# Optimization experiments

Measured on AMD Instinct MI355X. Metric: run time of the kernel, lower is better.

## Reference

```python
import jax, jax.numpy as jnp
import numpy as np

N = 100000
E = 1600000
C_IN = 128
C_OUT = 128
EPS = 1e-5


def setup_inputs() -> dict:
    key = jax.random.key(0)
    ks = jax.random.split(key, 8)
    x = jax.random.normal(ks[0], (N, C_IN), dtype=jnp.float32)
    edge_index = jax.random.randint(ks[1], (2, E), 0, N, dtype=jnp.int64)
    s_proj = 1.0 / np.sqrt(C_IN)
    s_out = 1.0 / np.sqrt(C_IN)
    W_proj = jax.random.uniform(ks[2], (C_IN, C_IN), jnp.float32, -s_proj, s_proj)
    b_proj = jax.random.uniform(ks[3], (C_IN,), jnp.float32, -s_proj, s_proj)
    W_l = jax.random.uniform(ks[4], (C_OUT, C_IN), jnp.float32, -s_out, s_out)
    b_l = jax.random.uniform(ks[5], (C_OUT,), jnp.float32, -s_out, s_out)
    W_r = jax.random.uniform(ks[6], (C_OUT, C_IN), jnp.float32, -s_out, s_out)
    gamma = jnp.ones((C_OUT,), jnp.float32)
    beta = jnp.zeros((C_OUT,), jnp.float32)
    return {"x": x, "edge_index": edge_index, "W_proj": W_proj, "b_proj": b_proj,
            "W_l": W_l, "b_l": b_l, "W_r": W_r, "gamma": gamma, "beta": beta}


def reference(x, edge_index, W_proj, b_proj, W_l, b_l, W_r, gamma, beta):
    # SAGEConv(project=True, aggr='sum'): project+ReLU source features per node,
    # gather along edges, scatter-sum at targets, then lin_l(agg) + lin_r(x_root).
    src, dst = edge_index[0], edge_index[1]
    h = jax.nn.relu(x @ W_proj.T + b_proj)            # [N, C_IN]
    msg = h[src]                                       # [E, C_IN] edge gather
    agg = jax.ops.segment_sum(msg, dst, num_segments=N)  # [N, C_IN]
    out = agg @ W_l.T + b_l + x @ W_r.T                # [N, C_OUT] (root uses unprojected x)
    # LayerNorm(c_out)
    mu = jnp.mean(out, axis=-1, keepdims=True)
    var = jnp.var(out, axis=-1, keepdims=True)
    return (out - mu) * jax.lax.rsqrt(var + EPS) * gamma + beta
```

## Files before the change

kernel.cpp:

```cpp
#include <hip/hip_runtime.h>
#include <stdint.h>

#define NN 100000
#define NE 1600000
#define C  128
#define NB 782
#define CAP 4096
#define SB_SHIFT 13
#define MB 782
#define P1B 250

typedef __attribute__((ext_vector_type(8))) short short8;
typedef __attribute__((ext_vector_type(4))) float f32x4;

__device__ __forceinline__ float bf2f(uint16_t u) {
  union { uint32_t u; float f; } v; v.u = ((uint32_t)u) << 16; return v.f;
}
__device__ __forceinline__ uint16_t f2bf(float f) {
  union { float f; uint32_t u; } v; v.f = f;
  uint32_t r = v.u + 0x7fffu + ((v.u >> 16) & 1u);
  return (uint16_t)(r >> 16);
}

__global__ __launch_bounds__(256) void cast3_k(
    const float* __restrict__ a, const float* __restrict__ b, const float* __restrict__ c,
    uint16_t* __restrict__ oa, uint16_t* __restrict__ ob, uint16_t* __restrict__ oc)
{
  int i = blockIdx.x * 256 + threadIdx.x;
  int which = i >> 12, j = i & 4095;
  const float* s = which == 0 ? a : (which == 1 ? b : c);
  uint16_t* d    = which == 0 ? oa : (which == 1 ? ob : oc);
  float4 v = ((const float4*)s)[j];
  uint2 p;
  p.x = (uint32_t)f2bf(v.x) | ((uint32_t)f2bf(v.y) << 16);
  p.y = (uint32_t)f2bf(v.z) | ((uint32_t)f2bf(v.w) << 16);
  ((uint2*)d)[j] = p;
}


__global__ __launch_bounds__(512) void fused_front_k(
    const float* __restrict__ x, const uint16_t* __restrict__ wpb,
    const float* __restrict__ bias, uint16_t* __restrict__ h,
    uint16_t* __restrict__ xb,
    const int* __restrict__ esrc, const int* __restrict__ edst,
    int* __restrict__ gcnt, uint32_t* __restrict__ ebuf)
{
  extern __shared__ uint8_t slds[];
  const int t = threadIdx.x;

  if (blockIdx.x < MB) {
#pragma unroll
    for (int q = 0; q < 4; ++q) {
      int ci = q * 512 + t;
      int c = ci >> 4, k16 = ci & 15;
      *(short8*)(slds + c * 256 + ((k16 ^ (c & 15)) << 4)) =
          *(const short8*)(wpb + ci * 8);
    }
    __syncthreads();

    const int w = t >> 6, lane = t & 63;
    const int tile_m = blockIdx.x * 128 + w * 16;
    if (tile_m >= NN) return;
    const int r16 = lane & 15, g = lane >> 4;

    short8 a[4];
    const float* xp = x + (size_t)(tile_m + r16) * C + g * 8;
    uint16_t* xbp = xb + (size_t)(tile_m + r16) * C + g * 8;
#pragma unroll
    for (int kk = 0; kk < 4; ++kk) {
      float4 u = *(const float4*)(xp + kk * 32);
      float4 v = *(const float4*)(xp + kk * 32 + 4);
      short8 av;
      av[0] = (short)f2bf(u.x); av[1] = (short)f2bf(u.y);
      av[2] = (short)f2bf(u.z); av[3] = (short)f2bf(u.w);
      av[4] = (short)f2bf(v.x); av[5] = (short)f2bf(v.y);
      av[6] = (short)f2bf(v.z); av[7] = (short)f2bf(v.w);
      a[kk] = av;
      *(short8*)(xbp + kk * 32) = av;
    }

#pragma unroll
    for (int nt = 0; nt < 8; ++nt) {
      f32x4 acc = {0.f, 0.f, 0.f, 0.f};
      const int c = nt * 16 + r16;
      const uint8_t* rb = slds + c * 256;
#pragma unroll
      for (int kk = 0; kk < 4; ++kk) {
        short8 b = *(const short8*)(rb + ((((kk << 2) + g) ^ (c & 15)) << 4));
        acc = __builtin_amdgcn_mfma_f32_16x16x32_bf16(a[kk], b, acc, 0, 0, 0);
      }
      const float bv = bias[c];
#pragma unroll
      for (int r = 0; r < 4; ++r) {
        int row = tile_m + g * 4 + r;
        float v = acc[r] + bv;
        v = v > 0.f ? v : 0.f;
        h[(size_t)row * C + c] = f2bf(v);
      }
    }
  } else {
    int* bh = (int*)slds;
    int* gb = bh + NB;
    const int blk = blockIdx.x - MB;
    const int base = blk * 6400;

    for (int i = t; i < NB; i += 512) bh[i] = 0;

    const int4* ed4 = (const int4*)(edst + base);
    const int4* es4 = (const int4*)(esrc + base);
    int4 dv[4], sv[4];
    bool val[4];
#pragma unroll
    for (int k = 0; k < 4; ++k) {
      int i = t + k * 512;
      val[k] = (i < 1600);
      if (val[k]) { dv[k] = ed4[i]; sv[k] = es4[i]; }
    }
    __syncthreads();

#pragma unroll
    for (int k = 0; k < 4; ++k) if (val[k]) {
      atomicAdd(&bh[dv[k].x >> 7], 1); atomicAdd(&bh[dv[k].y >> 7], 1);
      atomicAdd(&bh[dv[k].z >> 7], 1); atomicAdd(&bh[dv[k].w >> 7], 1);
    }
    __syncthreads();

    for (int i = t; i < NB; i += 512) {
      int c = bh[i];
      gb[i] = c ? atomicAdd(&gcnt[i], c) : 0;
      bh[i] = 0;
    }
    __syncthreads();

#define P1_SCATTER(d, s) do { \
      int bb = (d) >> 7; \
      int o = atomicAdd(&bh[bb], 1); \
      int pos = gb[bb] + o; \
      if (pos < CAP) ebuf[(size_t)bb * CAP + pos] = ((uint32_t)((d) & 127) << 17) | (uint32_t)(s); \
    } while (0)

#pragma unroll
    for (int k = 0; k < 4; ++k) if (val[k]) {
      P1_SCATTER(dv[k].x, sv[k].x); P1_SCATTER(dv[k].y, sv[k].y);
      P1_SCATTER(dv[k].z, sv[k].z); P1_SCATTER(dv[k].w, sv[k].w);
    }
#undef P1_SCATTER
  }
}

__global__ __launch_bounds__(1024) void scan_block_k(
    const int* __restrict__ in, int* __restrict__ out, int n)
{
  __shared__ int sm[1024];
  int t = threadIdx.x;
  int v = (t < n) ? in[t] : 0;
  sm[t] = v;
  __syncthreads();
  for (int off = 1; off < 1024; off <<= 1) {
    int x = (t >= off) ? sm[t - off] : 0;
    __syncthreads();
    sm[t] += x;
    __syncthreads();
  }
  if (t < n) out[t] = sm[t] - v;
}

__global__ __launch_bounds__(256) void phase2_k(
    const uint32_t* __restrict__ ebuf, const int* __restrict__ gcnt,
    const int* __restrict__ gbase, int* __restrict__ ssrc,
    int* __restrict__ start, int* __restrict__ deg)
{
  __shared__ uint32_t raw[CAP];
  __shared__ int lout[CAP];
  __shared__ int cnt2[128 * 16];
  __shared__ int nd[128];
  const int b = blockIdx.x, t = threadIdx.x;
  const int n0 = b * 128;
  int cnt = gcnt[b]; if (cnt > CAP) cnt = CAP;
  const int base = gbase[b];

  for (int i = t; i < 128 * 16; i += 256) cnt2[i] = 0;
  __syncthreads();
  for (int i = t; i < cnt; i += 256) {
    uint32_t v = ebuf[(size_t)b * CAP + i];
    raw[i] = v;
    atomicAdd(&cnt2[(v >> 17) * 16 + ((v & 0x1FFFFu) >> SB_SHIFT)], 1);
  }
  __syncthreads();

  int deg_t = 0;
  if (t < 128) {
#pragma unroll
    for (int i = 0; i < 16; ++i) deg_t += cnt2[t * 16 + i];
    nd[t] = deg_t;
  }
  __syncthreads();
  for (int off = 1; off < 128; off <<= 1) {
    int v = 0;
    if (t < 128 && t >= off) v = nd[t - off];
    __syncthreads();
    if (t < 128) nd[t] += v;
    __syncthreads();
  }
  if (t < 128) {
    int pref = nd[t] - deg_t;
    if (n0 + t < NN) { start[n0 + t] = base + pref; deg[n0 + t] = deg_t; }
    int run = pref;
#pragma unroll
    for (int i = 0; i < 16; ++i) { int c = cnt2[t * 16 + i]; cnt2[t * 16 + i] = run; run += c; }
  }
  __syncthreads();
  for (int i = t; i < cnt; i += 256) {
    uint32_t v = raw[i];
    int o = atomicAdd(&cnt2[(v >> 17) * 16 + ((v & 0x1FFFFu) >> SB_SHIFT)], 1);
    lout[o] = (int)(v & 0x1FFFFu);
  }
  __syncthreads();
  for (int i = t; i < cnt; i += 256) ssrc[base + i] = lout[i];
}

__global__ __launch_bounds__(256) void aggregate_k(
    const uint16_t* __restrict__ h, const int* __restrict__ ssrc,
    const int* __restrict__ start, const int* __restrict__ deg,
    uint16_t* __restrict__ agg)
{
  const int wid = (blockIdx.x * 256 + threadIdx.x) >> 6;
  if (wid >= NN) return;
  const int lane = threadIdx.x & 63;
  const int q = lane >> 4;
  const int l16 = lane & 15;
  const int s0 = start[wid];
  const int cnt = deg[wid];
  const size_t choff = (size_t)l16 * 8;
  float a[8];
#pragma unroll
  for (int i = 0; i < 8; ++i) a[i] = 0.f;

#define ACC8(v) do { \
    a[0] += bf2f((uint16_t)(v).x); a[1] += bf2f((uint16_t)((v).x >> 16)); \
    a[2] += bf2f((uint16_t)(v).y); a[3] += bf2f((uint16_t)((v).y >> 16)); \
    a[4] += bf2f((uint16_t)(v).z); a[5] += bf2f((uint16_t)((v).z >> 16)); \
    a[6] += bf2f((uint16_t)(v).w); a[7] += bf2f((uint16_t)((v).w >> 16)); \
  } while (0)

  int j = 0;
  for (; j + 16 <= cnt; j += 16) {
    int e0 = ssrc[s0 + j + q];
    int e1 = ssrc[s0 + j + 4 + q];
    int e2 = ssrc[s0 + j + 8 + q];
    int e3 = ssrc[s0 + j + 12 + q];
    uint4 v0 = *(const uint4*)(h + (size_t)e0 * C + choff);
    uint4 v1 = *(const uint4*)(h + (size_t)e1 * C + choff);
    uint4 v2 = *(const uint4*)(h + (size_t)e2 * C + choff);
    uint4 v3 = *(const uint4*)(h + (size_t)e3 * C + choff);
    ACC8(v0); ACC8(v1); ACC8(v2); ACC8(v3);
  }
  const int rem = cnt - j;
  if (rem > 0) {
    int i0 = (q      < rem) ? q      : 0;
    int i1 = (q + 4  < rem) ? q + 4  : 0;
    int i2 = (q + 8  < rem) ? q + 8  : 0;
    int i3 = (q + 12 < rem) ? q + 12 : 0;
    int e0 = ssrc[s0 + j + i0];
    int e1 = ssrc[s0 + j + i1];
    int e2 = ssrc[s0 + j + i2];
    int e3 = ssrc[s0 + j + i3];
    uint4 v0 = *(const uint4*)(h + (size_t)e0 * C + choff);
    uint4 v1 = *(const uint4*)(h + (size_t)e1 * C + choff);
    uint4 v2 = *(const uint4*)(h + (size_t)e2 * C + choff);
    uint4 v3 = *(const uint4*)(h + (size_t)e3 * C + choff);
    if (q < rem)      ACC8(v0);
    if (q + 4 < rem)  ACC8(v1);
    if (q + 8 < rem)  ACC8(v2);
    if (q + 12 < rem) ACC8(v3);
  }
#undef ACC8

#pragma unroll
  for (int i = 0; i < 8; ++i) {
    a[i] += __shfl_xor(a[i], 16, 64);
    a[i] += __shfl_xor(a[i], 32, 64);
  }
  if (q == 0) {
    uint4 p;
    p.x = (uint32_t)f2bf(a[0]) | ((uint32_t)f2bf(a[1]) << 16);
    p.y = (uint32_t)f2bf(a[2]) | ((uint32_t)f2bf(a[3]) << 16);
    p.z = (uint32_t)f2bf(a[4]) | ((uint32_t)f2bf(a[5]) << 16);
    p.w = (uint32_t)f2bf(a[6]) | ((uint32_t)f2bf(a[7]) << 16);
    *(uint4*)(agg + (size_t)wid * C + choff) = p;
  }
}

__global__ __launch_bounds__(512) void gemm_out_k(
    const uint16_t* __restrict__ aggb, const uint16_t* __restrict__ xb,
    const uint16_t* __restrict__ wlb, const uint16_t* __restrict__ wrb,
    const float* __restrict__ bl, const float* __restrict__ gamma,
    const float* __restrict__ beta, float* __restrict__ out)
{
  extern __shared__ uint8_t slds[];
  const int t = threadIdx.x;
#pragma unroll
  for (int q = 0; q < 4; ++q) {
    int ci = q * 512 + t;
    int c = ci >> 4, k16 = ci & 15;
    *(short8*)(slds + c * 256 + ((k16 ^ (c & 15)) << 4)) =
        *(const short8*)(wlb + ci * 8);
  }
#pragma unroll
  for (int q = 0; q < 4; ++q) {
    int ci = q * 512 + t;
    int c = ci >> 4, k16 = ci & 15;
    *(short8*)(slds + 32768 + c * 256 + ((k16 ^ (c & 15)) << 4)) =
        *(const short8*)(wrb + ci * 8);
  }
  __syncthreads();

  const int w = t >> 6, lane = t & 63;
  const int tile_m = blockIdx.x * 128 + w * 16;
  if (tile_m >= NN) return;
  const int r16 = lane & 15, g = lane >> 4;

  short8 a0[4], a1[4];
  const uint16_t* p0 = aggb + (size_t)(tile_m + r16) * C + g * 8;
  const uint16_t* p1 = xb   + (size_t)(tile_m + r16) * C + g * 8;
#pragma unroll
  for (int kk = 0; kk < 4; ++kk) {
    a0[kk] = *(const short8*)(p0 + kk * 32);
    a1[kk] = *(const short8*)(p1 + kk * 32);
  }

  f32x4 acc[8];
#pragma unroll
  for (int nt = 0; nt < 8; ++nt) {
    f32x4 c4 = {0.f, 0.f, 0.f, 0.f};
    const int c = nt * 16 + r16;
    const uint8_t* rbl = slds + c * 256;
    const uint8_t* rbr = slds + 32768 + c * 256;
#pragma unroll
    for (int kk = 0; kk < 4; ++kk) {
      short8 b = *(const short8*)(rbl + ((((kk << 2) + g) ^ (c & 15)) << 4));
      c4 = __builtin_amdgcn_mfma_f32_16x16x32_bf16(a0[kk], b, c4, 0, 0, 0);
    }
#pragma unroll
    for (int kk = 0; kk < 4; ++kk) {
      short8 b = *(const short8*)(rbr + ((((kk << 2) + g) ^ (c & 15)) << 4));
      c4 = __builtin_amdgcn_mfma_f32_16x16x32_bf16(a1[kk], b, c4, 0, 0, 0);
    }
    const float bv = bl[c];
#pragma unroll
    for (int r = 0; r < 4; ++r) c4[r] += bv;
    acc[nt] = c4;
  }

  float s1[4], s2[4];
#pragma unroll
  for (int r = 0; r < 4; ++r) { s1[r] = 0.f; s2[r] = 0.f; }
#pragma unroll
  for (int nt = 0; nt < 8; ++nt)
#pragma unroll
    for (int r = 0; r < 4; ++r) { float v = acc[nt][r]; s1[r] += v; s2[r] += v * v; }
#pragma unroll
  for (int m = 1; m <= 8; m <<= 1) {
#pragma unroll
    for (int r = 0; r < 4; ++r) {
      s1[r] += __shfl_xor(s1[r], m, 64);
      s2[r] += __shfl_xor(s2[r], m, 64);
    }
  }
  float mean[4], rstd[4];
#pragma unroll
  for (int r = 0; r < 4; ++r) {
    mean[r] = s1[r] * (1.f / C);
    float var = s2[r] * (1.f / C) - mean[r] * mean[r];
    rstd[r] = rsqrtf(var + 1e-5f);
  }
#pragma unroll
  for (int nt = 0; nt < 8; ++nt) {
    const int col = nt * 16 + r16;
    const float gmv = gamma[col], btv = beta[col];
#pragma unroll
    for (int r = 0; r < 4; ++r) {
      int row = tile_m + g * 4 + r;
      out[(size_t)row * C + col] = (acc[nt][r] - mean[r]) * rstd[r] * gmv + btv;
    }
  }
}

extern "C" void kernel_launch(void* const* d_in, const int* in_sizes, int n_in,
                              void* d_out, int out_size, void* d_ws, size_t ws_size,
                              hipStream_t stream)
{
  const float* x        = (const float*)d_in[0];
  const int* ei         = (const int*)d_in[1];
  const float* Wp       = (const float*)d_in[2];
  const float* bp       = (const float*)d_in[3];
  const float* Wl       = (const float*)d_in[4];
  const float* bl       = (const float*)d_in[5];
  const float* Wr       = (const float*)d_in[6];
  const float* gamma    = (const float*)d_in[7];
  const float* beta     = (const float*)d_in[8];
  float* out            = (float*)d_out;

  char* ws = (char*)d_ws;
  uint16_t* xb   = (uint16_t*)(ws + 0);
  uint16_t* h    = (uint16_t*)(ws + 25600000);
  uint16_t* aggb = (uint16_t*)(ws + 51200000);
  uint32_t* ebuf = (uint32_t*)(ws + 51200000);
  uint16_t* wpb  = (uint16_t*)(ws + 76800000);
  uint16_t* wlb  = (uint16_t*)(ws + 76832768);
  uint16_t* wrb  = (uint16_t*)(ws + 76865536);
  int* deg       = (int*)(ws + 76898304);
  int* start     = (int*)(ws + 77298304);
  int* gcnt      = (int*)(ws + 77698304);
  int* gbase     = (int*)(ws + 77702400);
  int* ssrc      = (int*)(ws + 78102400);

  const int* esrc = ei;
  const int* edst = ei + NE;

  hipMemsetAsync(gcnt, 0, NB * sizeof(int), stream);

  cast3_k<<<48, 256, 0, stream>>>(Wp, Wl, Wr, wpb, wlb, wrb);

  fused_front_k<<<MB + P1B, 512, 32768, stream>>>(
      x, wpb, bp, h, xb, esrc, edst, gcnt, ebuf);

  scan_block_k<<<1, 1024, 0, stream>>>(gcnt, gbase, NB);
  phase2_k<<<NB, 256, 0, stream>>>(ebuf, gcnt, gbase, ssrc, start, deg);

  aggregate_k<<<(NN + 3) / 4, 256, 0, stream>>>(h, ssrc, start, deg, aggb);

  gemm_out_k<<<MB, 512, 65536, stream>>>(aggb, xb, wlb, wrb, bl, gamma, beta, out);
}
```

Baseline: 136.5 us.

## Fuse aggregation with output GEMM and move root projection into front kernel

The root term x@W_r^T+b_l now runs in the front kernel next to the projection, reusing the same x fragments, and is stored as a bf16 buffer in place of the bf16 copy of x. Aggregation and the lin_l GEMM with LayerNorm are merged into one kernel. Each wave gathers 16 rows into an LDS tile, with each 16-lane group handling one node and 8 neighbours in flight, then runs MFMA against W_l held in LDS. This removes the agg round trip through global memory and one launch. In exchange the gather parallelism per node changes, the front kernel needs 64KB LDS, and the root term is now rounded to bf16.

Result: slower. 175.2 us (+28.4%).

```diff
diff --git a/kernel.cpp b/kernel.cpp
--- a/kernel.cpp
+++ b/kernel.cpp
@@ -40,8 +40,9 @@
 
 __global__ __launch_bounds__(512) void fused_front_k(
     const float* __restrict__ x, const uint16_t* __restrict__ wpb,
-    const float* __restrict__ bias, uint16_t* __restrict__ h,
-    uint16_t* __restrict__ xb,
+    const uint16_t* __restrict__ wrb,
+    const float* __restrict__ bp, const float* __restrict__ bl,
+    uint16_t* __restrict__ h, uint16_t* __restrict__ rb,
     const int* __restrict__ esrc, const int* __restrict__ edst,
     int* __restrict__ gcnt, uint32_t* __restrict__ ebuf)
 {
@@ -50,11 +51,12 @@
 
   if (blockIdx.x < MB) {
 #pragma unroll
-    for (int q = 0; q < 4; ++q) {
-      int ci = q * 512 + t;
+    for (int qq = 0; qq < 4; ++qq) {
+      int ci = qq * 512 + t;
       int c = ci >> 4, k16 = ci & 15;
-      *(short8*)(slds + c * 256 + ((k16 ^ (c & 15)) << 4)) =
-          *(const short8*)(wpb + ci * 8);
+      int slot = (k16 ^ (c & 15)) << 4;
+      *(short8*)(slds + c * 256 + slot)         = *(const short8*)(wpb + ci * 8);
+      *(short8*)(slds + 32768 + c * 256 + slot) = *(const short8*)(wrb + ci * 8);
     }
     __syncthreads();
 
@@ -63,9 +65,9 @@
     if (tile_m >= NN) return;
     const int r16 = lane & 15, g = lane >> 4;
 
+    int arow = tile_m + r16; if (arow >= NN) arow = NN - 1;
     short8 a[4];
-    const float* xp = x + (size_t)(tile_m + r16) * C + g * 8;
-    uint16_t* xbp = xb + (size_t)(tile_m + r16) * C + g * 8;
+    const float* xp = x + (size_t)arow * C + g * 8;
 #pragma unroll
     for (int kk = 0; kk < 4; ++kk) {
       float4 u = *(const float4*)(xp + kk * 32);
@@ -76,26 +78,31 @@
       av[4] = (short)f2bf(v.x); av[5] = (short)f2bf(v.y);
       av[6] = (short)f2bf(v.z); av[7] = (short)f2bf(v.w);
       a[kk] = av;
-      *(short8*)(xbp + kk * 32) = av;
     }
 
 #pragma unroll
     for (int nt = 0; nt < 8; ++nt) {
-      f32x4 acc = {0.f, 0.f, 0.f, 0.f};
+      f32x4 ap = {0.f, 0.f, 0.f, 0.f};
+      f32x4 ar = {0.f, 0.f, 0.f, 0.f};
       const int c = nt * 16 + r16;
-      const uint8_t* rb = slds + c * 256;
+      const uint8_t* rbp = slds + c * 256;
+      const uint8_t* rbr = slds + 32768 + c * 256;
 #pragma unroll
       for (int kk = 0; kk < 4; ++kk) {
-        short8 b = *(const short8*)(rb + ((((kk << 2) + g) ^ (c & 15)) << 4));
-        acc = __builtin_amdgcn_mfma_f32_16x16x32_bf16(a[kk], b, acc, 0, 0, 0);
+        int slot = (((kk << 2) + g) ^ (c & 15)) << 4;
+        ap = __builtin_amdgcn_mfma_f32_16x16x32_bf16(a[kk], *(const short8*)(rbp + slot), ap, 0, 0, 0);
+        ar = __builtin_amdgcn_mfma_f32_16x16x32_bf16(a[kk], *(const short8*)(rbr + slot), ar, 0, 0, 0);
       }
-      const float bv = bias[c];
-#pragma unroll
-      for (int r = 0; r < 4; ++r) {
-        int row = tile_m + g * 4 + r;
-        float v = acc[r] + bv;
-        v = v > 0.f ? v : 0.f;
-        h[(size_t)row * C + c] = f2bf(v);
+      const float bpv = bp[c], blv = bl[c];
+#pragma unroll
+      for (int rr = 0; rr < 4; ++rr) {
+        int row = tile_m + g * 4 + rr;
+        if (row < NN) {
+          float vh = ap[rr] + bpv;
+          vh = vh > 0.f ? vh : 0.f;
+          h[(size_t)row * C + c]  = f2bf(vh);
+          rb[(size_t)row * C + c] = f2bf(ar[rr] + blv);
+        }
       }
     }
   } else {
@@ -219,22 +226,28 @@
   for (int i = t; i < cnt; i += 256) ssrc[base + i] = lout[i];
 }
 
-__global__ __launch_bounds__(256) void aggregate_k(
+__global__ __launch_bounds__(256) void fused_back_k(
     const uint16_t* __restrict__ h, const int* __restrict__ ssrc,
     const int* __restrict__ start, const int* __restrict__ deg,
-    uint16_t* __restrict__ agg)
-{
-  const int wid = (blockIdx.x * 256 + threadIdx.x) >> 6;
-  if (wid >= NN) return;
-  const int lane = threadIdx.x & 63;
-  const int q = lane >> 4;
-  const int l16 = lane & 15;
-  const int s0 = start[wid];
-  const int cnt = deg[wid];
-  const size_t choff = (size_t)l16 * 8;
-  float a[8];
-#pragma unroll
-  for (int i = 0; i < 8; ++i) a[i] = 0.f;
+    const uint16_t* __restrict__ wlb, const uint16_t* __restrict__ rb,
+    const float* __restrict__ gamma, const float* __restrict__ beta,
+    float* __restrict__ out)
+{
+  __shared__ uint8_t wl[32768];
+  __shared__ uint8_t tile[16384];
+  const int t = threadIdx.x;
+
+#pragma unroll
+  for (int qq = 0; qq < 8; ++qq) {
+    int ci = qq * 256 + t;
+    int c = ci >> 4, k16 = ci & 15;
+    *(short8*)(wl + c * 256 + ((k16 ^ (c & 15)) << 4)) = *(const short8*)(wlb + ci * 8);
+  }
+  __syncthreads();
+
+  const int w = t >> 6, lane = t & 63;
+  const int q = lane >> 4, l16 = lane & 15;
+  const int row_base = blockIdx.x * 64 + w * 16;
 
 #define ACC8(v) do { \
     a[0] += bf2f((uint16_t)(v).x); a[1] += bf2f((uint16_t)((v).x >> 16)); \
@@ -243,145 +256,98 @@
     a[6] += bf2f((uint16_t)(v).w); a[7] += bf2f((uint16_t)((v).w >> 16)); \
   } while (0)
 
-  int j = 0;
-  for (; j + 16 <= cnt; j += 16) {
-    int e0 = ssrc[s0 + j + q];
-    int e1 = ssrc[s0 + j + 4 + q];
-    int e2 = ssrc[s0 + j + 8 + q];
-    int e3 = ssrc[s0 + j + 12 + q];
-    uint4 v0 = *(const uint4*)(h + (size_t)e0 * C + choff);
-    uint4 v1 = *(const uint4*)(h + (size_t)e1 * C + choff);
-    uint4 v2 = *(const uint4*)(h + (size_t)e2 * C + choff);
-    uint4 v3 = *(const uint4*)(h + (size_t)e3 * C + choff);
-    ACC8(v0); ACC8(v1); ACC8(v2); ACC8(v3);
-  }
-  const int rem = cnt - j;
-  if (rem > 0) {
-    int i0 = (q      < rem) ? q      : 0;
-    int i1 = (q + 4  < rem) ? q + 4  : 0;
-    int i2 = (q + 8  < rem) ? q + 8  : 0;
-    int i3 = (q + 12 < rem) ? q + 12 : 0;
-    int e0 = ssrc[s0 + j + i0];
-    int e1 = ssrc[s0 + j + i1];
-    int e2 = ssrc[s0 + j + i2];
-    int e3 = ssrc[s0 + j + i3];
-    uint4 v0 = *(const uint4*)(h + (size_t)e0 * C + choff);
-    uint4 v1 = *(const uint4*)(h + (size_t)e1 * C + choff);
-    uint4 v2 = *(const uint4*)(h + (size_t)e2 * C + choff);
-    uint4 v3 = *(const uint4*)(h + (size_t)e3 * C + choff);
-    if (q < rem)      ACC8(v0);
-    if (q + 4 < rem)  ACC8(v1);
-    if (q + 8 < rem)  ACC8(v2);
-    if (q + 12 < rem) ACC8(v3);
-  }
-#undef ACC8
-
-#pragma unroll
-  for (int i = 0; i < 8; ++i) {
-    a[i] += __shfl_xor(a[i], 16, 64);
-    a[i] += __shfl_xor(a[i], 32, 64);
-  }
-  if (q == 0) {
+#pragma unroll
+  for (int m = 0; m < 4; ++m) {
+    const int rrow = m * 4 + q;
+    const int n = row_base + rrow;
+    const int cnt = (n < NN) ? deg[n] : 0;
+    const int s0  = (n < NN) ? start[n] : 0;
+    float a[8];
+#pragma unroll
+    for (int i = 0; i < 8; ++i) a[i] = 0.f;
+
+    for (int j = 0; j < cnt; j += 8) {
+      int e[8];
+#pragma unroll
+      for (int k = 0; k < 8; ++k) {
+        int idx = j + k; if (idx >= cnt) idx = cnt - 1;
+        e[k] = ssrc[s0 + idx];
+      }
+      uint4 vv[8];
+#pragma unroll
+      for (int k = 0; k < 8; ++k)
+        vv[k] = *(const uint4*)(h + (size_t)e[k] * C + (size_t)l16 * 8);
+#pragma unroll
+      for (int k = 0; k < 8; ++k)
+        if (j + k < cnt) ACC8(vv[k]);
+    }
     uint4 p;
     p.x = (uint32_t)f2bf(a[0]) | ((uint32_t)f2bf(a[1]) << 16);
     p.y = (uint32_t)f2bf(a[2]) | ((uint32_t)f2bf(a[3]) << 16);
     p.z = (uint32_t)f2bf(a[4]) | ((uint32_t)f2bf(a[5]) << 16);
     p.w = (uint32_t)f2bf(a[6]) | ((uint32_t)f2bf(a[7]) << 16);
-    *(uint4*)(agg + (size_t)wid * C + choff) = p;
-  }
-}
-
-__global__ __launch_bounds__(512) void gemm_out_k(
-    const uint16_t* __restrict__ aggb, const uint16_t* __restrict__ xb,
-    const uint16_t* __restrict__ wlb, const uint16_t* __restrict__ wrb,
-    const float* __restrict__ bl, const float* __restrict__ gamma,
-    const float* __restrict__ beta, float* __restrict__ out)
-{
-  extern __shared__ uint8_t slds[];
-  const int t = threadIdx.x;
-#pragma unroll
-  for (int q = 0; q < 4; ++q) {
-    int ci = q * 512 + t;
-    int c = ci >> 4, k16 = ci & 15;
-    *(short8*)(slds + c * 256 + ((k16 ^ (c & 15)) << 4)) =
-        *(const short8*)(wlb + ci * 8);
-  }
-#pragma unroll
-  for (int q = 0; q < 4; ++q) {
-    int ci = q * 512 + t;
-    int c = ci >> 4, k16 = ci & 15;
-    *(short8*)(slds + 32768 + c * 256 + ((k16 ^ (c & 15)) << 4)) =
-        *(const short8*)(wrb + ci * 8);
-  }
-  __syncthreads();
-
-  const int w = t >> 6, lane = t & 63;
-  const int tile_m = blockIdx.x * 128 + w * 16;
-  if (tile_m >= NN) return;
+    *(uint4*)(tile + (size_t)(w * 16 + rrow) * 256 + ((l16 ^ rrow) << 4)) = p;
+  }
+#undef ACC8
+
   const int r16 = lane & 15, g = lane >> 4;
-
-  short8 a0[4], a1[4];
-  const uint16_t* p0 = aggb + (size_t)(tile_m + r16) * C + g * 8;
-  const uint16_t* p1 = xb   + (size_t)(tile_m + r16) * C + g * 8;
-#pragma unroll
-  for (int kk = 0; kk < 4; ++kk) {
-    a0[kk] = *(const short8*)(p0 + kk * 32);
-    a1[kk] = *(const short8*)(p1 + kk * 32);
-  }
+  short8 af[4];
+#pragma unroll
+  for (int kk = 0; kk < 4; ++kk)
+    af[kk] = *(const short8*)(tile + (size_t)(w * 16 + r16) * 256 +
+                              ((((kk << 2) + g) ^ r16) << 4));
 
   f32x4 acc[8];
 #pragma unroll
   for (int nt = 0; nt < 8; ++nt) {
     f32x4 c4 = {0.f, 0.f, 0.f, 0.f};
     const int c = nt * 16 + r16;
-    const uint8_t* rbl = slds + c * 256;
-    const uint8_t* rbr = slds + 32768 + c * 256;
+    const uint8_t* rbl = wl + c * 256;
 #pragma unroll
     for (int kk = 0; kk < 4; ++kk) {
       short8 b = *(const short8*)(rbl + ((((kk << 2) + g) ^ (c & 15)) << 4));
-      c4 = __builtin_amdgcn_mfma_f32_16x16x32_bf16(a0[kk], b, c4, 0, 0, 0);
-    }
-#pragma unroll
-    for (int kk = 0; kk < 4; ++kk) {
-      short8 b = *(const short8*)(rbr + ((((kk << 2) + g) ^ (c & 15)) << 4));
-      c4 = __builtin_amdgcn_mfma_f32_16x16x32_bf16(a1[kk], b, c4, 0, 0, 0);
-    }
-    const float bv = bl[c];
-#pragma unroll
-    for (int r = 0; r < 4; ++r) c4[r] += bv;
+      c4 = __builtin_amdgcn_mfma_f32_16x16x32_bf16(af[kk], b, c4, 0, 0, 0);
+    }
+#pragma unroll
+    for (int rr = 0; rr < 4; ++rr) {
+      int row = row_base + g * 4 + rr;
+      float rv = (row < NN) ? bf2f(rb[(size_t)row * C + c]) : 0.f;
+      c4[rr] += rv;
+    }
     acc[nt] = c4;
   }
 
   float s1[4], s2[4];
 #pragma unroll
-  for (int r = 0; r < 4; ++r) { s1[r] = 0.f; s2[r] = 0.f; }
+  for (int rr = 0; rr < 4; ++rr) { s1[rr] = 0.f; s2[rr] = 0.f; }
 #pragma unroll
   for (int nt = 0; nt < 8; ++nt)
 #pragma unroll
-    for (int r = 0; r < 4; ++r) { float v = acc[nt][r]; s1[r] += v; s2[r] += v * v; }
-#pragma unroll
-  for (int m = 1; m <= 8; m <<= 1) {
-#pragma unroll
-    for (int r = 0; r < 4; ++r) {
-      s1[r] += __shfl_xor(s1[r], m, 64);
-      s2[r] += __shfl_xor(s2[r], m, 64);
+    for (int rr = 0; rr < 4; ++rr) { float v = acc[nt][rr]; s1[rr] += v; s2[rr] += v * v; }
+#pragma unroll
+  for (int msk = 1; msk <= 8; msk <<= 1) {
+#pragma unroll
+    for (int rr = 0; rr < 4; ++rr) {
+      s1[rr] += __shfl_xor(s1[rr], msk, 64);
+      s2[rr] += __shfl_xor(s2[rr], msk, 64);
     }
   }
   float mean[4], rstd[4];
 #pragma unroll
-  for (int r = 0; r < 4; ++r) {
-    mean[r] = s1[r] * (1.f / C);
-    float var = s2[r] * (1.f / C) - mean[r] * mean[r];
-    rstd[r] = rsqrtf(var + 1e-5f);
+  for (int rr = 0; rr < 4; ++rr) {
+    mean[rr] = s1[rr] * (1.f / C);
+    float var = s2[rr] * (1.f / C) - mean[rr] * mean[rr];
+    rstd[rr] = rsqrtf(var + 1e-5f);
   }
 #pragma unroll
   for (int nt = 0; nt < 8; ++nt) {
     const int col = nt * 16 + r16;
     const float gmv = gamma[col], btv = beta[col];
 #pragma unroll
-    for (int r = 0; r < 4; ++r) {
-      int row = tile_m + g * 4 + r;
-      out[(size_t)row * C + col] = (acc[nt][r] - mean[r]) * rstd[r] * gmv + btv;
+    for (int rr = 0; rr < 4; ++rr) {
+      int row = row_base + g * 4 + rr;
+      if (row < NN)
+        out[(size_t)row * C + col] = (acc[nt][rr] - mean[rr]) * rstd[rr] * gmv + btv;
     }
   }
 }
@@ -402,9 +368,8 @@
   float* out            = (float*)d_out;
 
   char* ws = (char*)d_ws;
-  uint16_t* xb   = (uint16_t*)(ws + 0);
+  uint16_t* rb   = (uint16_t*)(ws + 0);
   uint16_t* h    = (uint16_t*)(ws + 25600000);
-  uint16_t* aggb = (uint16_t*)(ws + 51200000);
   uint32_t* ebuf = (uint32_t*)(ws + 51200000);
   uint16_t* wpb  = (uint16_t*)(ws + 76800000);
   uint16_t* wlb  = (uint16_t*)(ws + 76832768);
@@ -422,13 +387,12 @@
 
   cast3_k<<<48, 256, 0, stream>>>(Wp, Wl, Wr, wpb, wlb, wrb);
 
-  fused_front_k<<<MB + P1B, 512, 32768, stream>>>(
-      x, wpb, bp, h, xb, esrc, edst, gcnt, ebuf);
+  fused_front_k<<<MB + P1B, 512, 65536, stream>>>(
+      x, wpb, wrb, bp, bl, h, rb, esrc, edst, gcnt, ebuf);
 
   scan_block_k<<<1, 1024, 0, stream>>>(gcnt, gbase, NB);
   phase2_k<<<NB, 256, 0, stream>>>(ebuf, gcnt, gbase, ssrc, start, deg);
 
-  aggregate_k<<<(NN + 3) / 4, 256, 0, stream>>>(h, ssrc, start, deg, aggb);
-
-  gemm_out_k<<<MB, 512, 65536, stream>>>(aggb, xb, wlb, wrb, bl, gamma, beta, out);
-}
+  fused_back_k<<<(NN + 63) / 64, 256, 0, stream>>>(
+      h, ssrc, start, deg, wlb, rb, gamma, beta, out);
+}
```
